# Kernel tuning notes

Measured on AMD Instinct MI355X. Metric: run time of the kernel, lower is better.

The kernel has to match this reference:

```python
import jax, jax.numpy as jnp
import numpy as np

B, C, O, H, W, K, PAD = 8, 256, 256, 56, 56, 3, 1
KK = K * K


def setup_inputs() -> dict:
    key = jax.random.key(0)
    k1, k2, k3, k4 = jax.random.split(key, 4)
    x = jax.random.normal(k1, (B, C, H, W), jnp.float32)
    # offset conv params (original zero-inits; small random used so sampling is off-grid)
    w_off = jax.random.normal(k2, (2 * KK, C, K, K), jnp.float32) * 0.01
    b_off = jnp.zeros((2 * KK,), jnp.float32)
    # deformable conv weight/bias (torchvision DeformConv2d default has bias)
    w_dcn = jax.random.normal(k3, (O, C, K, K), jnp.float32) * (1.0 / np.sqrt(C * KK))
    b_dcn = jax.random.normal(k4, (O,), jnp.float32) * 0.01
    return dict(x=x, w_off=w_off, b_off=b_off, w_dcn=w_dcn, b_dcn=b_dcn)


def _conv3x3(x, w, b):
    y = jax.lax.conv_general_dilated(
        x, w, window_strides=(1, 1), padding=((PAD, PAD), (PAD, PAD)),
        dimension_numbers=('NCHW', 'OIHW', 'NCHW'))
    return y + b[None, :, None, None]


def _deform_sample(x, py, px):
    """Zero-padded bilinear gather of x[B,C,H,W] at (py,px)[B,KK,H,W] -> [B,C,KK,H,W]."""
    xf = x.reshape(B, C, H * W)
    y0 = jnp.floor(py)
    x0 = jnp.floor(px)
    fy = py - y0
    fx = px - x0
    val = 0.0
    for dy, dx, wgt in ((0, 0, (1 - fy) * (1 - fx)),
                        (0, 1, (1 - fy) * fx),
                        (1, 0, fy * (1 - fx)),
                        (1, 1, fy * fx)):
        yc = y0 + dy
        xc = x0 + dx
        ok = (yc >= 0) & (yc < H) & (xc >= 0) & (xc < W)  # zero-padding outside
        yi = jnp.clip(yc, 0, H - 1).astype(jnp.int32)
        xi = jnp.clip(xc, 0, W - 1).astype(jnp.int32)
        idx = (yi * W + xi).reshape(B, 1, KK * H * W)  # broadcast over channel dim
        g = jnp.take_along_axis(xf, idx, axis=2).reshape(B, C, KK, H, W)
        val = val + (wgt * ok)[:, None] * g
    return val


def reference(x, w_off, b_off, w_dcn, b_dcn):
    # 1) predict per-pixel offsets: [B, 2*K*K, H, W], torchvision layout (dy,dx) pairs
    off = _conv3x3(x, w_off, b_off)
    dy = off[:, 0::2]  # [B, KK, H, W]
    dx = off[:, 1::2]
    # 2) sampling grid: base pixel + kernel tap offset + learned offset
    ky = (jnp.arange(KK) // K - PAD).astype(jnp.float32)
    kx = (jnp.arange(KK) % K - PAD).astype(jnp.float32)
    hgrid = jnp.arange(H, dtype=jnp.float32)
    wgrid = jnp.arange(W, dtype=jnp.float32)
    py = hgrid[None, None, :, None] + ky[None, :, None, None] + dy
    px = wgrid[None, None, None, :] + kx[None, :, None, None] + dx
    # 3) bilinear gather + weighted accumulation over (c, kernel tap)
    val = _deform_sample(x, py, px)  # [B, C, KK, H, W]
    out = jnp.einsum('bckhw,ock->bohw', val, w_dcn.reshape(O, C, KK))
    return out + b_dcn[None, :, None, None]
```

## Files before the change

kernel.cpp:

```cpp
#include <hip/hip_runtime.h>

#define B_  8
#define C_  256
#define O_  256
#define H_  56
#define W_  56
#define HW_ 3136
#define KK_ 9
#define CK_ 2304
#define NKC 72

typedef __bf16    bf16x8 __attribute__((ext_vector_type(8)));
typedef float     f32x4  __attribute__((ext_vector_type(4)));

__device__ __forceinline__ void async16(const void* gsrc_lane, void* lds_uniform) {
    __builtin_amdgcn_global_load_lds(
        (const __attribute__((address_space(1))) unsigned int*)gsrc_lane,
        (__attribute__((address_space(3))) unsigned int*)lds_uniform, 16, 0, 0);
}

__device__ __forceinline__ int swz4(int r) { return (r & 3) ^ ((r >> 2) & 3); }

__device__ __forceinline__ float blo(unsigned u) {
    return __builtin_bit_cast(float, u << 16);
}
__device__ __forceinline__ float bhi(unsigned u) {
    return __builtin_bit_cast(float, u & 0xffff0000u);
}
__device__ __forceinline__ unsigned pkbf(float lo, float hi) {
    unsigned short a = __builtin_bit_cast(unsigned short, (__bf16)lo);
    unsigned short b = __builtin_bit_cast(unsigned short, (__bf16)hi);
    return (unsigned)a | ((unsigned)b << 16);
}

__device__ __forceinline__ uint4 bilin4(uint4 c00, uint4 c01, uint4 c10, uint4 c11,
                                        float4 wg) {
    uint4 o;
    float lo_, hi_;
    lo_ = wg.x*blo(c00.x) + wg.y*blo(c01.x) + wg.z*blo(c10.x) + wg.w*blo(c11.x);
    hi_ = wg.x*bhi(c00.x) + wg.y*bhi(c01.x) + wg.z*bhi(c10.x) + wg.w*bhi(c11.x);
    o.x = pkbf(lo_, hi_);
    lo_ = wg.x*blo(c00.y) + wg.y*blo(c01.y) + wg.z*blo(c10.y) + wg.w*blo(c11.y);
    hi_ = wg.x*bhi(c00.y) + wg.y*bhi(c01.y) + wg.z*bhi(c10.y) + wg.w*bhi(c11.y);
    o.y = pkbf(lo_, hi_);
    lo_ = wg.x*blo(c00.z) + wg.y*blo(c01.z) + wg.z*blo(c10.z) + wg.w*blo(c11.z);
    hi_ = wg.x*bhi(c00.z) + wg.y*bhi(c01.z) + wg.z*bhi(c10.z) + wg.w*bhi(c11.z);
    o.z = pkbf(lo_, hi_);
    lo_ = wg.x*blo(c00.w) + wg.y*blo(c01.w) + wg.z*blo(c10.w) + wg.w*blo(c11.w);
    hi_ = wg.x*bhi(c00.w) + wg.y*bhi(c01.w) + wg.z*bhi(c10.w) + wg.w*bhi(c11.w);
    o.w = pkbf(lo_, hi_);
    return o;
}

__global__ __launch_bounds__(256) void k_buildA(const float* __restrict__ w,
                                                unsigned short* __restrict__ wA) {
    int d  = blockIdx.x * 256 + threadIdx.x;
    int kc = d >> 13;
    int rd = d & 8191;
    int m  = rd >> 5;
    int pos = rd & 31;
    int q  = (pos >> 3) ^ swz4(m);
    int kl = q * 8 + (pos & 7);
    int gk = kc * 32 + kl;
    int tap = gk >> 8, c = gk & 255;
    __bf16 v = (__bf16)w[m * CK_ + c * KK_ + tap];
    wA[d] = __builtin_bit_cast(unsigned short, v);
}

__global__ __launch_bounds__(256) void k_transx(const float* __restrict__ x,
                                                unsigned short* __restrict__ xT) {
    __shared__ float s[64][65];
    int bt   = blockIdx.x;
    int c64  = bt & 3;
    int hw64 = (bt >> 2) % 49;
    int b    = bt / 196;
    int tx = threadIdx.x & 63;
    int ty = threadIdx.x >> 6;
#pragma unroll
    for (int i = 0; i < 16; ++i)
        s[i * 4 + ty][tx] =
            x[((size_t)(b * 256 + c64 * 64 + i * 4 + ty)) * HW_ + hw64 * 64 + tx];
    __syncthreads();
#pragma unroll
    for (int i = 0; i < 16; ++i) {
        float v = s[tx][i * 4 + ty];
        xT[((size_t)b * HW_ + hw64 * 64 + i * 4 + ty) * 256 + c64 * 64 + tx] =
            __builtin_bit_cast(unsigned short, (__bf16)v);
    }
}

__global__ __launch_bounds__(512) void k_offc1(const float* __restrict__ x,
                                               const float* __restrict__ w_off,
                                               float* __restrict__ part) {
    __shared__ float partial[8][64][18];
    int t  = threadIdx.x;
    int p  = t & 63;
    int cg = __builtin_amdgcn_readfirstlane(t >> 6);
    int orig = blockIdx.x;
    int blk  = (orig & 7) * 196 + (orig >> 3);
    int sl   = blk & 3;
    int un   = blk >> 2;
    int b    = un / 49;
    int pos0 = (un % 49) * 64;
    int pos  = pos0 + p;
    int h = pos / W_;
    int w = pos % W_;
    const float* xb = x + (size_t)b * C_ * HW_;

    float acc[18];
#pragma unroll
    for (int i = 0; i < 18; ++i) acc[i] = 0.f;

    for (int cc = 0; cc < 8; ++cc) {
        int c = sl * 64 + cg * 8 + cc;
        const float* xp = xb + c * HW_;
        float v[9];
#pragma unroll
        for (int dh = -1; dh <= 1; ++dh)
#pragma unroll
            for (int dw = -1; dw <= 1; ++dw) {
                int hh = h + dh, ww = w + dw;
                bool ok = (hh >= 0) & (hh < H_) & (ww >= 0) & (ww < W_);
                v[(dh + 1) * 3 + dw + 1] = ok ? xp[hh * W_ + ww] : 0.f;
            }
        const float* wc = w_off + c * KK_;
#pragma unroll
        for (int oc = 0; oc < 18; ++oc) {
            const float* wr = wc + oc * CK_;
#pragma unroll
            for (int k = 0; k < KK_; ++k)
                acc[oc] = fmaf(v[k], wr[k], acc[oc]);
        }
    }
#pragma unroll
    for (int oc = 0; oc < 18; ++oc) partial[cg][p][oc] = acc[oc];
    __syncthreads();

    float* po = part + (size_t)sl * (B_ * 18 * HW_);
    for (int e = t; e < 64 * 18; e += 512) {
        int oc = e >> 6;
        int pp = e & 63;
        float s = 0.f;
#pragma unroll
        for (int g = 0; g < 8; ++g) s += partial[g][pp][oc];
        po[((size_t)b * 18 + oc) * HW_ + pos0 + pp] = s;
    }
}

__global__ __launch_bounds__(256) void k_offc2(const float* __restrict__ part,
                                               const float* __restrict__ b_off,
                                               float* __restrict__ off) {
    int i = blockIdx.x * 256 + threadIdx.x;
    const int NP = B_ * 18 * HW_;
    int oc = (i / HW_) % 18;
    off[i] = part[i] + part[i + NP] + part[i + 2 * NP] + part[i + 3 * NP]
           + b_off[oc];
}

__device__ __forceinline__ void fstage(
    int s, int chNext, bool issueA, bool prod, bool reload,
    const char* xb, const char* gA0,
    __bf16 (*s_a)[8192], __bf16 (*s_b)[2048],
    int (*s_id)[64][4], float (*s_w)[64][4],
    int4& id, float4& wg,
    int n, int tc, int sc, int wv, int lid, int quad, int swz, int lo,
    f32x4 (&acc)[4][4]) {

    if (reload) {
        int tp1 = (s + 1) >> 3;
        id = *(const int4*)s_id[tp1][n];
        wg = *(const float4*)s_w[tp1][n];
    }
    uint4 c00, c01, c10, c11;
    if (prod) {
        const char* p = xb + chNext * 64 + tc * 16;
        c00 = *(const uint4*)(p + id.x);
        c01 = *(const uint4*)(p + id.y);
        c10 = *(const uint4*)(p + id.z);
        c11 = *(const uint4*)(p + id.w);
    }
    if (issueA) {
        const char* ga = gA0 + (size_t)(s + 2) * 16384;
        char* la = (char*)s_a[(s + 2) % 3];
#pragma unroll
        for (int j = 0; j < 4; ++j)
            async16(ga + wv * 4096 + j * 1024 + lo, la + wv * 4096 + j * 1024);
    }
    asm volatile("s_waitcnt vmcnt(12)" ::: "memory");

    const bf16x8* pa = (const bf16x8*)s_a[s % 3];
    const bf16x8* pb = (const bf16x8*)s_b[s & 1];
    bf16x8 af[4], bv[4];
#pragma unroll
    for (int mi = 0; mi < 4; ++mi)
        af[mi] = pa[(wv * 64 + mi * 16 + lid) * 4 + (quad ^ swz)];
#pragma unroll
    for (int ni = 0; ni < 4; ++ni)
        bv[ni] = pb[(ni * 16 + lid) * 4 + (quad ^ swz)];

    __builtin_amdgcn_s_setprio(1);
#pragma unroll
    for (int mi = 0; mi < 4; ++mi)
#pragma unroll
        for (int ni = 0; ni < 4; ++ni)
            acc[mi][ni] = __builtin_amdgcn_mfma_f32_16x16x32_bf16(
                af[mi], bv[ni], acc[mi][ni], 0, 0, 0);
    __builtin_amdgcn_s_setprio(0);

    if (prod) {
        uint4 o = bilin4(c00, c01, c10, c11, wg);
        *(uint4*)((char*)s_b[(s & 1) ^ 1] + n * 64 + sc * 16) = o;
    }
    asm volatile("s_waitcnt lgkmcnt(0)" ::: "memory");
    __builtin_amdgcn_s_barrier();
    __builtin_amdgcn_sched_barrier(0);
}

__global__ __launch_bounds__(256, 2) void k_fused(
    const unsigned short* __restrict__ xT,
    const float* __restrict__ off,
    const __bf16* __restrict__ wA,
    const float* __restrict__ b_dcn,
    float* __restrict__ out) {

    __shared__ __bf16 s_a[3][8192];
    __shared__ __bf16 s_b[2][2048];
    __shared__ int    s_id[KK_][64][4];
    __shared__ float  s_w [KK_][64][4];

    int bid  = blockIdx.x;
    int g    = (bid & 7) * 49 + (bid >> 3);
    int b    = g / 49;
    int pos0 = (g % 49) * 64;
    int t    = threadIdx.x;
    int lane = t & 63;
    int wv   = t >> 6;
    int lid  = lane & 15;
    int quad = lane >> 4;
    int swz  = swz4(lid);

    for (int e = t; e < KK_ * 64; e += 256) {
        int k = e >> 6, n = e & 63;
        int pos = pos0 + n;
        int h = pos / W_, w = pos % W_;
        float dy = off[((size_t)b * 18 + 2 * k) * HW_ + pos];
        float dx = off[((size_t)b * 18 + 2 * k + 1) * HW_ + pos];
        float py = (float)(h + k / 3 - 1) + dy;
        float px = (float)(w + k % 3 - 1) + dx;
        float y0f = floorf(py), x0f = floorf(px);
        float fy = py - y0f, fx = px - x0f;
        int y0 = (int)y0f, x0 = (int)x0f;
        int y1 = y0 + 1,   x1 = x0 + 1;
        float oy0 = (y0 >= 0 && y0 < H_) ? 1.f : 0.f;
        float oy1 = (y1 >= 0 && y1 < H_) ? 1.f : 0.f;
        float ox0 = (x0 >= 0 && x0 < W_) ? 1.f : 0.f;
        float ox1 = (x1 >= 0 && x1 < W_) ? 1.f : 0.f;
        int y0c = min(max(y0, 0), H_ - 1), y1c = min(max(y1, 0), H_ - 1);
        int x0c = min(max(x0, 0), W_ - 1), x1c = min(max(x1, 0), W_ - 1);
        s_id[k][n][0] = (y0c * W_ + x0c) * 512;
        s_id[k][n][1] = (y0c * W_ + x1c) * 512;
        s_id[k][n][2] = (y1c * W_ + x0c) * 512;
        s_id[k][n][3] = (y1c * W_ + x1c) * 512;
        s_w[k][n][0] = (1.f - fy) * (1.f - fx) * oy0 * ox0;
        s_w[k][n][1] = (1.f - fy) * fx         * oy0 * ox1;
        s_w[k][n][2] = fy * (1.f - fx)         * oy1 * ox0;
        s_w[k][n][3] = fy * fx                 * oy1 * ox1;
    }
    __syncthreads();

    int n  = t >> 2;
    int tc = t & 3;
    int sc = tc ^ swz4(n);
    const char* xb  = (const char*)(xT + (size_t)b * HW_ * 256);
    const char* gA0 = (const char*)wA;
    int lo = lane * 16;

    f32x4 acc[4][4];
#pragma unroll
    for (int mi = 0; mi < 4; ++mi)
#pragma unroll
        for (int ni = 0; ni < 4; ++ni)
            acc[mi][ni] = (f32x4)(0.f);

    int4   id = *(const int4*)s_id[0][n];
    float4 wg = *(const float4*)s_w[0][n];
    {
        const char* p = xb + tc * 16;
        uint4 c00 = *(const uint4*)(p + id.x);
        uint4 c01 = *(const uint4*)(p + id.y);
        uint4 c10 = *(const uint4*)(p + id.z);
        uint4 c11 = *(const uint4*)(p + id.w);
#pragma unroll
        for (int ss = 0; ss < 2; ++ss) {
            const char* ga = gA0 + (size_t)ss * 16384;
            char* la = (char*)s_a[ss];
#pragma unroll
            for (int j = 0; j < 4; ++j)
                async16(ga + wv * 4096 + j * 1024 + lo, la + wv * 4096 + j * 1024);
        }
        uint4 o = bilin4(c00, c01, c10, c11, wg);
        *(uint4*)((char*)s_b[0] + n * 64 + sc * 16) = o;
    }
    asm volatile("s_waitcnt lgkmcnt(0)" ::: "memory");
    __builtin_amdgcn_s_barrier();
    __builtin_amdgcn_sched_barrier(0);

    for (int tap = 0; tap < 8; ++tap) {
        int s0 = tap * 8;
#pragma unroll
        for (int i = 0; i < 8; ++i)
            fstage(s0 + i, (i + 1) & 7, true, true, i == 7,
                   xb, gA0, s_a, s_b, s_id, s_w, id, wg,
                   n, tc, sc, wv, lid, quad, swz, lo, acc);
    }
#pragma unroll
    for (int i = 0; i < 8; ++i)
        fstage(64 + i, (i + 1) & 7, i < 6, i < 7, false,
               xb, gA0, s_a, s_b, s_id, s_w, id, wg,
               n, tc, sc, wv, lid, quad, swz, lo, acc);

#pragma unroll
    for (int mi = 0; mi < 4; ++mi) {
#pragma unroll
        for (int r = 0; r < 4; ++r) {
            int m = wv * 64 + mi * 16 + quad * 4 + r;
            float bias = b_dcn[m];
            float* po = out + ((size_t)b * O_ + m) * HW_ + pos0 + lid;
#pragma unroll
            for (int ni = 0; ni < 4; ++ni)
                po[ni * 16] = acc[mi][ni][r] + bias;
        }
    }
}

extern "C" void kernel_launch(void* const* d_in, const int* in_sizes, int n_in,
                              void* d_out, int out_size, void* d_ws, size_t ws_size,
                              hipStream_t stream) {
    const float* x     = (const float*)d_in[0];
    const float* w_off = (const float*)d_in[1];
    const float* b_off = (const float*)d_in[2];
    const float* w_dcn = (const float*)d_in[3];
    const float* b_dcn = (const float*)d_in[4];
    float* out = (float*)d_out;

    const size_t offBytes  = (size_t)451584 * 4;
    const size_t wABytes   = (size_t)589824 * 2;
    const size_t xTBytes   = (size_t)B_ * HW_ * 256 * 2;
    float*          off  = (float*)d_ws;
    unsigned short* wA   = (unsigned short*)((char*)d_ws + offBytes);
    unsigned short* xT   = (unsigned short*)((char*)d_ws + offBytes + wABytes);
    float*          part = (float*)((char*)d_ws + offBytes + wABytes + xTBytes);

    k_buildA <<<2304, 256, 0, stream>>>(w_dcn, wA);
    k_transx <<<1568, 256, 0, stream>>>(x, xT);
    k_offc1  <<<1568, 512, 0, stream>>>(x, w_off, part);
    k_offc2  <<<1764, 256, 0, stream>>>(part, b_off, off);
    k_fused  <<<392,  256, 0, stream>>>(xT, off, (const __bf16*)wA, b_dcn, out);
}
```

Baseline: 203.8 us.

## Load weight fragments directly into registers and deepen gather prefetch to two stages

After: 217.6 us. 1.07x slower.

```diff
diff --git a/kernel.cpp b/kernel.cpp
--- a/kernel.cpp
+++ b/kernel.cpp
@@ -12,12 +12,6 @@
 
 typedef __bf16    bf16x8 __attribute__((ext_vector_type(8)));
 typedef float     f32x4  __attribute__((ext_vector_type(4)));
-
-__device__ __forceinline__ void async16(const void* gsrc_lane, void* lds_uniform) {
-    __builtin_amdgcn_global_load_lds(
-        (const __attribute__((address_space(1))) unsigned int*)gsrc_lane,
-        (__attribute__((address_space(3))) unsigned int*)lds_uniform, 16, 0, 0);
-}
 
 __device__ __forceinline__ int swz4(int r) { return (r & 3) ^ ((r >> 2) & 3); }
 
@@ -157,43 +151,42 @@
            + b_off[oc];
 }
 
+template<bool ISSUEC, bool ISSUEA, bool PROD, bool RELID, bool RELWG>
 __device__ __forceinline__ void fstage(
-    int s, int chNext, bool issueA, bool prod, bool reload,
+    int s, int chNext,
     const char* xb, const char* gA0,
-    __bf16 (*s_a)[8192], __bf16 (*s_b)[2048],
+    __bf16 (*s_b)[2048],
     int (*s_id)[64][4], float (*s_w)[64][4],
     int4& id, float4& wg,
-    int n, int tc, int sc, int wv, int lid, int quad, int swz, int lo,
+    uint4 (&cUse)[4], uint4 (&cFill)[4],
+    bf16x8 (&afUse)[4], bf16x8 (&afFill)[4],
+    int aoffBase,
+    int n, int tc, int sc, int lid, int quad, int swz,
     f32x4 (&acc)[4][4]) {
 
-    if (reload) {
-        int tp1 = (s + 1) >> 3;
-        id = *(const int4*)s_id[tp1][n];
-        wg = *(const float4*)s_w[tp1][n];
-    }
-    uint4 c00, c01, c10, c11;
-    if (prod) {
+    if (RELID) {
+        id = *(const int4*)s_id[(s + 2) >> 3][n];
+    }
+    if (RELWG) {
+        wg = *(const float4*)s_w[(s + 1) >> 3][n];
+    }
+    if (ISSUEC) {
         const char* p = xb + chNext * 64 + tc * 16;
-        c00 = *(const uint4*)(p + id.x);
-        c01 = *(const uint4*)(p + id.y);
-        c10 = *(const uint4*)(p + id.z);
-        c11 = *(const uint4*)(p + id.w);
-    }
-    if (issueA) {
-        const char* ga = gA0 + (size_t)(s + 2) * 16384;
-        char* la = (char*)s_a[(s + 2) % 3];
-#pragma unroll
-        for (int j = 0; j < 4; ++j)
-            async16(ga + wv * 4096 + j * 1024 + lo, la + wv * 4096 + j * 1024);
-    }
-    asm volatile("s_waitcnt vmcnt(12)" ::: "memory");
-
-    const bf16x8* pa = (const bf16x8*)s_a[s % 3];
+        cFill[0] = *(const uint4*)(p + id.x);
+        cFill[1] = *(const uint4*)(p + id.y);
+        cFill[2] = *(const uint4*)(p + id.z);
+        cFill[3] = *(const uint4*)(p + id.w);
+    }
+    if (ISSUEA) {
+        const char* ga = gA0 + (size_t)(s + 1) * 16384 + aoffBase;
+        afFill[0] = *(const bf16x8*)(ga);
+        afFill[1] = *(const bf16x8*)(ga + 1024);
+        afFill[2] = *(const bf16x8*)(ga + 2048);
+        afFill[3] = *(const bf16x8*)(ga + 3072);
+    }
+
     const bf16x8* pb = (const bf16x8*)s_b[s & 1];
-    bf16x8 af[4], bv[4];
-#pragma unroll
-    for (int mi = 0; mi < 4; ++mi)
-        af[mi] = pa[(wv * 64 + mi * 16 + lid) * 4 + (quad ^ swz)];
+    bf16x8 bv[4];
 #pragma unroll
     for (int ni = 0; ni < 4; ++ni)
         bv[ni] = pb[(ni * 16 + lid) * 4 + (quad ^ swz)];
@@ -204,11 +197,11 @@
 #pragma unroll
         for (int ni = 0; ni < 4; ++ni)
             acc[mi][ni] = __builtin_amdgcn_mfma_f32_16x16x32_bf16(
-                af[mi], bv[ni], acc[mi][ni], 0, 0, 0);
+                afUse[mi], bv[ni], acc[mi][ni], 0, 0, 0);
     __builtin_amdgcn_s_setprio(0);
 
-    if (prod) {
-        uint4 o = bilin4(c00, c01, c10, c11, wg);
+    if (PROD) {
+        uint4 o = bilin4(cUse[0], cUse[1], cUse[2], cUse[3], wg);
         *(uint4*)((char*)s_b[(s & 1) ^ 1] + n * 64 + sc * 16) = o;
     }
     asm volatile("s_waitcnt lgkmcnt(0)" ::: "memory");
@@ -216,14 +209,13 @@
     __builtin_amdgcn_sched_barrier(0);
 }
 
-__global__ __launch_bounds__(256, 2) void k_fused(
+__global__ __launch_bounds__(256, 3) void k_fused(
     const unsigned short* __restrict__ xT,
     const float* __restrict__ off,
     const __bf16* __restrict__ wA,
     const float* __restrict__ b_dcn,
     float* __restrict__ out) {
 
-    __shared__ __bf16 s_a[3][8192];
     __shared__ __bf16 s_b[2][2048];
     __shared__ int    s_id[KK_][64][4];
     __shared__ float  s_w [KK_][64][4];
@@ -273,7 +265,7 @@
     int sc = tc ^ swz4(n);
     const char* xb  = (const char*)(xT + (size_t)b * HW_ * 256);
     const char* gA0 = (const char*)wA;
-    int lo = lane * 16;
+    int aoffBase = (wv * 64 + lid) * 64 + (quad ^ swz) * 16;
 
     f32x4 acc[4][4];
 #pragma unroll
@@ -284,21 +276,27 @@
 
     int4   id = *(const int4*)s_id[0][n];
     float4 wg = *(const float4*)s_w[0][n];
+    uint4  cA[4], cB[4];
+    bf16x8 afA[4], afB[4];
+
     {
-        const char* p = xb + tc * 16;
-        uint4 c00 = *(const uint4*)(p + id.x);
-        uint4 c01 = *(const uint4*)(p + id.y);
-        uint4 c10 = *(const uint4*)(p + id.z);
-        uint4 c11 = *(const uint4*)(p + id.w);
-#pragma unroll
-        for (int ss = 0; ss < 2; ++ss) {
-            const char* ga = gA0 + (size_t)ss * 16384;
-            char* la = (char*)s_a[ss];
-#pragma unroll
-            for (int j = 0; j < 4; ++j)
-                async16(ga + wv * 4096 + j * 1024 + lo, la + wv * 4096 + j * 1024);
-        }
-        uint4 o = bilin4(c00, c01, c10, c11, wg);
+        const char* p0 = xb + tc * 16;
+        uint4 c0[4];
+        c0[0] = *(const uint4*)(p0 + id.x);
+        c0[1] = *(const uint4*)(p0 + id.y);
+        c0[2] = *(const uint4*)(p0 + id.z);
+        c0[3] = *(const uint4*)(p0 + id.w);
+        const char* ga = gA0 + aoffBase;
+        afA[0] = *(const bf16x8*)(ga);
+        afA[1] = *(const bf16x8*)(ga + 1024);
+        afA[2] = *(const bf16x8*)(ga + 2048);
+        afA[3] = *(const bf16x8*)(ga + 3072);
+        const char* p1 = xb + 64 + tc * 16;
+        cA[0] = *(const uint4*)(p1 + id.x);
+        cA[1] = *(const uint4*)(p1 + id.y);
+        cA[2] = *(const uint4*)(p1 + id.z);
+        cA[3] = *(const uint4*)(p1 + id.w);
+        uint4 o = bilin4(c0[0], c0[1], c0[2], c0[3], wg);
         *(uint4*)((char*)s_b[0] + n * 64 + sc * 16) = o;
     }
     asm volatile("s_waitcnt lgkmcnt(0)" ::: "memory");
@@ -307,17 +305,23 @@
 
     for (int tap = 0; tap < 8; ++tap) {
         int s0 = tap * 8;
-#pragma unroll
-        for (int i = 0; i < 8; ++i)
-            fstage(s0 + i, (i + 1) & 7, true, true, i == 7,
-                   xb, gA0, s_a, s_b, s_id, s_w, id, wg,
-                   n, tc, sc, wv, lid, quad, swz, lo, acc);
-    }
-#pragma unroll
-    for (int i = 0; i < 8; ++i)
-        fstage(64 + i, (i + 1) & 7, i < 6, i < 7, false,
-               xb, gA0, s_a, s_b, s_id, s_w, id, wg,
-               n, tc, sc, wv, lid, quad, swz, lo, acc);
+        fstage<true, true, true, false, false>(s0 + 0, 2, xb, gA0, s_b, s_id, s_w, id, wg, cA, cB, afA, afB, aoffBase, n, tc, sc, lid, quad, swz, acc);
+        fstage<true, true, true, false, false>(s0 + 1, 3, xb, gA0, s_b, s_id, s_w, id, wg, cB, cA, afB, afA, aoffBase, n, tc, sc, lid, quad, swz, acc);
+        fstage<true, true, true, false, false>(s0 + 2, 4, xb, gA0, s_b, s_id, s_w, id, wg, cA, cB, afA, afB, aoffBase, n, tc, sc, lid, quad, swz, acc);
+        fstage<true, true, true, false, false>(s0 + 3, 5, xb, gA0, s_b, s_id, s_w, id, wg, cB, cA, afB, afA, aoffBase, n, tc, sc, lid, quad, swz, acc);
+        fstage<true, true, true, false, false>(s0 + 4, 6, xb, gA0, s_b, s_id, s_w, id, wg, cA, cB, afA, afB, aoffBase, n, tc, sc, lid, quad, swz, acc);
+        fstage<true, true, true, false, false>(s0 + 5, 7, xb, gA0, s_b, s_id, s_w, id, wg, cB, cA, afB, afA, aoffBase, n, tc, sc, lid, quad, swz, acc);
+        fstage<true, true, true, true,  false>(s0 + 6, 0, xb, gA0, s_b, s_id, s_w, id, wg, cA, cB, afA, afB, aoffBase, n, tc, sc, lid, quad, swz, acc);
+        fstage<true, true, true, false, true >(s0 + 7, 1, xb, gA0, s_b, s_id, s_w, id, wg, cB, cA, afB, afA, aoffBase, n, tc, sc, lid, quad, swz, acc);
+    }
+    fstage<true,  true,  true,  false, false>(64, 2, xb, gA0, s_b, s_id, s_w, id, wg, cA, cB, afA, afB, aoffBase, n, tc, sc, lid, quad, swz, acc);
+    fstage<true,  true,  true,  false, false>(65, 3, xb, gA0, s_b, s_id, s_w, id, wg, cB, cA, afB, afA, aoffBase, n, tc, sc, lid, quad, swz, acc);
+    fstage<true,  true,  true,  false, false>(66, 4, xb, gA0, s_b, s_id, s_w, id, wg, cA, cB, afA, afB, aoffBase, n, tc, sc, lid, quad, swz, acc);
+    fstage<true,  true,  true,  false, false>(67, 5, xb, gA0, s_b, s_id, s_w, id, wg, cB, cA, afB, afA, aoffBase, n, tc, sc, lid, quad, swz, acc);
+    fstage<true,  true,  true,  false, false>(68, 6, xb, gA0, s_b, s_id, s_w, id, wg, cA, cB, afA, afB, aoffBase, n, tc, sc, lid, quad, swz, acc);
+    fstage<true,  true,  true,  false, false>(69, 7, xb, gA0, s_b, s_id, s_w, id, wg, cB, cA, afB, afA, aoffBase, n, tc, sc, lid, quad, swz, acc);
+    fstage<false, true,  true,  false, false>(70, 0, xb, gA0, s_b, s_id, s_w, id, wg, cA, cB, afA, afB, aoffBase, n, tc, sc, lid, quad, swz, acc);
+    fstage<false, false, false, false, false>(71, 1, xb, gA0, s_b, s_id, s_w, id, wg, cB, cA, afB, afA, aoffBase, n, tc, sc, lid, quad, swz, acc);
 
 #pragma unroll
     for (int mi = 0; mi < 4; ++mi) {
```
